# Kernel tuning notes

Hardware: AMD Instinct MI355X
Metric: run time of the kernel (lower is better)

Reference implementation:

```python
import jax, jax.numpy as jnp
import numpy as np

TAU = 0.07
EPS = 1e-12  # matches torch F.normalize clamp_min eps


def setup_inputs() -> dict:
    key = jax.random.key(0)
    k1, k2 = jax.random.split(key)
    feat = jax.random.normal(k1, (4, 64, 512, 512), dtype=jnp.float32)
    gt = jax.random.randint(k2, (4, 19, 512, 512), 0, 2, dtype=jnp.int32)
    return {"feat": feat, "gt": gt}


def reference(feat, gt):
    # feat: [b, c, h, w], gt: [b, k, h, w] multi-hot in {0,1}
    mask = (gt == 1).astype(feat.dtype)                      # [b,k,h,w]
    num_pos = mask.sum()

    # Scatter-sum class prototypes: k0[k] = sum of feat at positive pixels of class k
    k0 = jnp.einsum('bkhw,bchw->kc', mask, feat)             # [k,c]
    k0n = k0 / jnp.maximum(jnp.linalg.norm(k0, axis=1, keepdims=True), EPS)

    # Per-pixel L2-normalized features over channel dim
    fn = feat / jnp.maximum(jnp.linalg.norm(feat, axis=1, keepdims=True), EPS)

    # Cosine similarity to every prototype, temperature-scaled softmax NLL over classes
    logits = jnp.einsum('kc,bchw->bkhw', k0n, fn) / TAU      # [b,k,h,w]
    logp = jax.nn.log_softmax(logits, axis=1)

    # Sum NLL over all (pixel, class) positive pairs; a pixel positive for
    # multiple classes contributes once per class, exactly like the loop.
    loss = -(mask * logp).sum() / num_pos
    return loss
```

## Files before the change

### kernel.cpp

```cpp
#include <hip/hip_runtime.h>
#include <cstdint>
#include <cstddef>

#define HW    262144
#define C     64
#define K     19
#define NPIX  1048576
#define TAUINV (1.0f / 0.07f)
#define EPS   1e-12f

#define T1    128
#define NT1   (NPIX / T1)
#define TPB1  (HW / T1)
#define G1    2048


__device__ __forceinline__ float wave_reduce_f32(float v) {
#pragma unroll
    for (int off = 32; off; off >>= 1) v += __shfl_down(v, off);
    return v;
}

__device__ __forceinline__ unsigned wave_reduce_u32(unsigned v) {
#pragma unroll
    for (int off = 32; off; off >>= 1) v += __shfl_down(v, off);
    return v;
}

__device__ __forceinline__ void k1_prefetch(
    int tile, const float* __restrict__ feat, const int* __restrict__ gt,
    int tid, float4 f[8], unsigned* mpf)
{
    const int b   = tile >> 11;
    const int hw0 = (tile & (TPB1 - 1)) << 7;
    const float* fb = feat + (size_t)b * C * HW + hw0;
#pragma unroll
    for (int i = 0; i < 8; ++i) {
        const int v  = tid + (i << 8);
        const int c  = v >> 5;
        const int p0 = (v & 31) << 2;
        f[i] = *(const float4*)(fb + (size_t)c * HW + p0);
    }
    if (tid < T1) {
        const int* gp = gt + (size_t)b * K * HW + hw0 + tid;
        unsigned m = 0;
#pragma unroll
        for (int k = 0; k < K; ++k)
            m |= (gp[(size_t)k * HW] == 1) ? (1u << k) : 0u;
        *mpf = m;
    }
}

__global__ __launch_bounds__(256) void k1_proto(
    const float* __restrict__ feat, const int* __restrict__ gt,
    unsigned* __restrict__ pm,
    float* __restrict__ k0, unsigned* __restrict__ num_pos)
{
    __shared__ float    sf[64][129];
    __shared__ unsigned msk[T1];
    const int tid  = threadIdx.x;
    const int lane = tid & 63;
    const int wv   = tid >> 6;

    float acc[K];
#pragma unroll
    for (int k = 0; k < K; ++k) acc[k] = 0.0f;
    unsigned npos = 0;

    float4   f[8];
    unsigned mpf = 0;
    int tile = blockIdx.x;
    if (tile < NT1) k1_prefetch(tile, feat, gt, tid, f, &mpf);

    for (; tile < NT1; ) {
        if (tid < T1) {
            msk[tid] = mpf;
            if (pm) pm[(size_t)tile * T1 + tid] = mpf;
            npos += __popc(mpf);
        }
#pragma unroll
        for (int i = 0; i < 8; ++i) {
            const int v  = tid + (i << 8);
            const int c  = v >> 5;
            const int p0 = (v & 31) << 2;
            sf[c][p0 + 0] = f[i].x; sf[c][p0 + 1] = f[i].y;
            sf[c][p0 + 2] = f[i].z; sf[c][p0 + 3] = f[i].w;
        }
        __syncthreads();

        const int nxt = tile + G1;
        if (nxt < NT1) k1_prefetch(nxt, feat, gt, tid, f, &mpf);

#pragma unroll 4
        for (int p = 0; p < 32; ++p) {
            const int pp = (wv << 5) + p;
            const float    fv = sf[lane][pp];
            const unsigned m  = msk[pp];
#pragma unroll
            for (int k = 0; k < K; ++k) {
                const int s = ((int)(m << (31 - k))) >> 31;
                acc[k] += __int_as_float(s & __float_as_int(fv));
            }
        }
        __syncthreads();
        tile = nxt;
    }

    float* red = &sf[0][0];
    if (wv > 0) {
#pragma unroll
        for (int k = 0; k < K; ++k)
            red[(wv - 1) * (K * 64) + k * 64 + lane] = acc[k];
    }
    __syncthreads();
    if (wv == 0) {
#pragma unroll
        for (int k = 0; k < K; ++k) {
            const float v = acc[k]
                + red[0 * (K * 64) + k * 64 + lane]
                + red[1 * (K * 64) + k * 64 + lane]
                + red[2 * (K * 64) + k * 64 + lane];
            atomicAdd(&k0[k * 64 + lane], v);
        }
    }
    const unsigned np = wave_reduce_u32(npos);
    if (lane == 0) atomicAdd(num_pos, np);
}

__global__ __launch_bounds__(256) void k2_norm(
    const float* __restrict__ k0, float* __restrict__ k0n)
{
    __shared__ float rn[K];
    const int tid  = threadIdx.x;
    const int lane = tid & 63;
    const int wv   = tid >> 6;
    for (int cls = wv; cls < K; cls += 4) {
        const float v = k0[cls * 64 + lane];
        const float s = wave_reduce_f32(v * v);
        if (lane == 0) rn[cls] = 1.0f / fmaxf(sqrtf(s), EPS);
    }
    __syncthreads();
    for (int i = tid; i < K * 64; i += 256) k0n[i] = k0[i] * rn[i >> 6];
}

__global__ __launch_bounds__(256) void k3_loss(
    const float* __restrict__ feat, const int* __restrict__ gt,
    const unsigned* __restrict__ pm, const float* __restrict__ k0n,
    float* __restrict__ loss_sum)
{
    __shared__ __align__(16) float w[K * 64];
    const int tid = threadIdx.x;
    for (int i = tid; i < K * 64; i += 256) w[i] = k0n[i];
    __syncthreads();

    const int px0 = (blockIdx.x * 256 + tid) << 2;
    const int b   = px0 >> 18;
    const int hw  = px0 & (HW - 1);
    const float* fb = feat + (size_t)b * C * HW + hw;

    unsigned marr[4];
    if (pm) {
        const uint4 mv = *(const uint4*)(pm + px0);
        marr[0] = mv.x; marr[1] = mv.y; marr[2] = mv.z; marr[3] = mv.w;
    } else {
        marr[0] = marr[1] = marr[2] = marr[3] = 0;
        const int* gp = gt + (size_t)b * K * HW + hw;
#pragma unroll
        for (int k = 0; k < K; ++k) {
            const int4 g4 = *(const int4*)(gp + (size_t)k * HW);
            marr[0] |= (g4.x == 1) ? (1u << k) : 0u;
            marr[1] |= (g4.y == 1) ? (1u << k) : 0u;
            marr[2] |= (g4.z == 1) ? (1u << k) : 0u;
            marr[3] |= (g4.w == 1) ? (1u << k) : 0u;
        }
    }

    float4 dot[K];
#pragma unroll
    for (int k = 0; k < K; ++k) dot[k] = make_float4(0.f, 0.f, 0.f, 0.f);
    float4 ss = make_float4(0.f, 0.f, 0.f, 0.f);

    float4 f[8];
#pragma unroll
    for (int j = 0; j < 8; ++j)
        f[j] = *(const float4*)(fb + (size_t)j * HW);

#pragma unroll
    for (int cg = 0; cg < 64; cg += 8) {
        float4 g[8];
        if (cg + 8 < 64) {
#pragma unroll
            for (int j = 0; j < 8; ++j)
                g[j] = *(const float4*)(fb + (size_t)(cg + 8 + j) * HW);
        }
#pragma unroll
        for (int j = 0; j < 8; ++j) {
            const float4 fv = f[j];
            ss.x = fmaf(fv.x, fv.x, ss.x); ss.y = fmaf(fv.y, fv.y, ss.y);
            ss.z = fmaf(fv.z, fv.z, ss.z); ss.w = fmaf(fv.w, fv.w, ss.w);
        }
#pragma unroll
        for (int k = 0; k < K; ++k) {
            const float4 wa = *(const float4*)&w[k * 64 + cg];
            const float4 wb = *(const float4*)&w[k * 64 + cg + 4];
            float4 d = dot[k];
            d.x = fmaf(f[0].x, wa.x, d.x); d.y = fmaf(f[0].y, wa.x, d.y);
            d.z = fmaf(f[0].z, wa.x, d.z); d.w = fmaf(f[0].w, wa.x, d.w);
            d.x = fmaf(f[1].x, wa.y, d.x); d.y = fmaf(f[1].y, wa.y, d.y);
            d.z = fmaf(f[1].z, wa.y, d.z); d.w = fmaf(f[1].w, wa.y, d.w);
            d.x = fmaf(f[2].x, wa.z, d.x); d.y = fmaf(f[2].y, wa.z, d.y);
            d.z = fmaf(f[2].z, wa.z, d.z); d.w = fmaf(f[2].w, wa.z, d.w);
            d.x = fmaf(f[3].x, wa.w, d.x); d.y = fmaf(f[3].y, wa.w, d.y);
            d.z = fmaf(f[3].z, wa.w, d.z); d.w = fmaf(f[3].w, wa.w, d.w);
            d.x = fmaf(f[4].x, wb.x, d.x); d.y = fmaf(f[4].y, wb.x, d.y);
            d.z = fmaf(f[4].z, wb.x, d.z); d.w = fmaf(f[4].w, wb.x, d.w);
            d.x = fmaf(f[5].x, wb.y, d.x); d.y = fmaf(f[5].y, wb.y, d.y);
            d.z = fmaf(f[5].z, wb.y, d.z); d.w = fmaf(f[5].w, wb.y, d.w);
            d.x = fmaf(f[6].x, wb.z, d.x); d.y = fmaf(f[6].y, wb.z, d.y);
            d.z = fmaf(f[6].z, wb.z, d.z); d.w = fmaf(f[6].w, wb.z, d.w);
            d.x = fmaf(f[7].x, wb.w, d.x); d.y = fmaf(f[7].y, wb.w, d.y);
            d.z = fmaf(f[7].z, wb.w, d.z); d.w = fmaf(f[7].w, wb.w, d.w);
            dot[k] = d;
        }
        if (cg + 8 < 64) {
#pragma unroll
            for (int j = 0; j < 8; ++j) f[j] = g[j];
        }
    }

    float ls = 0.0f;
    float* dp = (float*)&dot[0];
    const float* sp = (const float*)&ss;
#pragma unroll
    for (int comp = 0; comp < 4; ++comp) {
        const float sc = TAUINV / fmaxf(sqrtf(sp[comp]), EPS);
        float mx = -1e30f;
#pragma unroll
        for (int k = 0; k < K; ++k) {
            dp[k * 4 + comp] *= sc;
            mx = fmaxf(mx, dp[k * 4 + comp]);
        }
        float se = 0.0f;
#pragma unroll
        for (int k = 0; k < K; ++k) se += expf(dp[k * 4 + comp] - mx);
        const float logZ = mx + logf(se);
        const unsigned m = marr[comp];
        ls += (float)__popc(m) * logZ;
#pragma unroll
        for (int k = 0; k < K; ++k) {
            const int s = ((int)(m << (31 - k))) >> 31;
            ls -= __int_as_float(s & __float_as_int(dp[k * 4 + comp]));
        }
    }

    ls = wave_reduce_f32(ls);
    if ((tid & 63) == 0) atomicAdd(loss_sum, ls);
}

__global__ void k4_final(const float* __restrict__ loss_sum,
                         const unsigned* __restrict__ num_pos,
                         float* __restrict__ out)
{
    out[0] = loss_sum[0] / (float)num_pos[0];
}

extern "C" void kernel_launch(void* const* d_in, const int* in_sizes, int n_in,
                              void* d_out, int out_size, void* d_ws, size_t ws_size,
                              hipStream_t stream)
{
    const float* feat = (const float*)d_in[0];
    const int*   gt   = (const int*)d_in[1];
    float*       out  = (float*)d_out;

    char* ws = (char*)d_ws;
    unsigned* num_pos  = (unsigned*)(ws + 0);
    float*    loss_sum = (float*)(ws + 4);
    float*    k0       = (float*)(ws + 64);
    float*    k0n      = (float*)(ws + 8192);
    unsigned* pm       = nullptr;
    if (ws_size >= 65536 + sizeof(unsigned) * (size_t)NPIX)
        pm = (unsigned*)(ws + 65536);

    hipMemsetAsync(d_ws, 0, 16384, stream);

    k1_proto<<<G1, 256, 0, stream>>>(feat, gt, pm, k0, num_pos);
    k2_norm <<<1,  256, 0, stream>>>(k0, k0n);
    k3_loss <<<NPIX / 1024, 256, 0, stream>>>(feat, gt, pm, k0n, loss_sum);
    k4_final<<<1, 1, 0, stream>>>(loss_sum, num_pos, out);
}
```

Before: 562.1 us.

## Compute class prototypes with bf16 MFMA using hi/lo split of features

The prototype scatter-sum kernel is rewritten so each wave takes 32-pixel chunks and computes the mask-by-feature product with 16x16x32 bf16 MFMA instructions. The masks become bf16 0/1 A operands, and each fp32 feature is split into high and low bf16 parts so the sum stays close to fp32. This replaces the scalar masked-add loop over 19 classes and the LDS transpose staging. The pixel-mask buffer is now always used, with no fallback when the workspace is small. This risks an out-of-bounds write if the workspace is too small and a small loss of precision from the two-term bf16 split.

Result: faster. 536.5 us (-4.5%).

```diff
diff --git a/kernel.cpp b/kernel.cpp
--- a/kernel.cpp
+++ b/kernel.cpp
@@ -9,138 +9,144 @@
 #define TAUINV (1.0f / 0.07f)
 #define EPS   1e-12f
 
-#define T1    128
-#define NT1   (NPIX / T1)
-#define TPB1  (HW / T1)
-#define G1    2048
-
+#define NCHUNK (NPIX / 32)
+#define CPB    8192
+#define G1     1024
+
+
+typedef __attribute__((ext_vector_type(8))) short bf16x8;
+typedef __attribute__((ext_vector_type(4))) float f32x4;
 
 __device__ __forceinline__ float wave_reduce_f32(float v) {
 #pragma unroll
     for (int off = 32; off; off >>= 1) v += __shfl_down(v, off);
     return v;
 }
-
 __device__ __forceinline__ unsigned wave_reduce_u32(unsigned v) {
 #pragma unroll
     for (int off = 32; off; off >>= 1) v += __shfl_down(v, off);
     return v;
 }
 
-__device__ __forceinline__ void k1_prefetch(
-    int tile, const float* __restrict__ feat, const int* __restrict__ gt,
-    int tid, float4 f[8], unsigned* mpf)
-{
-    const int b   = tile >> 11;
-    const int hw0 = (tile & (TPB1 - 1)) << 7;
-    const float* fb = feat + (size_t)b * C * HW + hw0;
-#pragma unroll
-    for (int i = 0; i < 8; ++i) {
-        const int v  = tid + (i << 8);
-        const int c  = v >> 5;
-        const int p0 = (v & 31) << 2;
-        f[i] = *(const float4*)(fb + (size_t)c * HW + p0);
-    }
-    if (tid < T1) {
-        const int* gp = gt + (size_t)b * K * HW + hw0 + tid;
-        unsigned m = 0;
-#pragma unroll
-        for (int k = 0; k < K; ++k)
-            m |= (gp[(size_t)k * HW] == 1) ? (1u << k) : 0u;
-        *mpf = m;
-    }
+__device__ __forceinline__ void split1(float f, short& h, short& l) {
+    const unsigned u  = __float_as_uint(f);
+    const unsigned hb = (u + 0x7FFFu + ((u >> 16) & 1u)) & 0xFFFF0000u;
+    h = (short)(hb >> 16);
+    const float lo = f - __uint_as_float(hb);
+    const unsigned v = __float_as_uint(lo);
+    l = (short)((v + 0x7FFFu + ((v >> 16) & 1u)) >> 16);
 }
 
 __global__ __launch_bounds__(256) void k1_proto(
     const float* __restrict__ feat, const int* __restrict__ gt,
     unsigned* __restrict__ pm,
-    float* __restrict__ k0, unsigned* __restrict__ num_pos)
-{
-    __shared__ float    sf[64][129];
-    __shared__ unsigned msk[T1];
+    float* __restrict__ k0p, unsigned* __restrict__ num_pos)
+{
+    __shared__ float red[32 * 64];
     const int tid  = threadIdx.x;
     const int lane = tid & 63;
     const int wv   = tid >> 6;
-
-    float acc[K];
-#pragma unroll
-    for (int k = 0; k < K; ++k) acc[k] = 0.0f;
+    const int q    = lane >> 4;
+    const int n    = lane & 15;
+    const int q8   = q << 3;
+
+    f32x4 acc[2][4];
+#pragma unroll
+    for (int mt = 0; mt < 2; ++mt)
+#pragma unroll
+        for (int nt = 0; nt < 4; ++nt)
+            acc[mt][nt] = (f32x4){0.f, 0.f, 0.f, 0.f};
     unsigned npos = 0;
 
-    float4   f[8];
-    unsigned mpf = 0;
-    int tile = blockIdx.x;
-    if (tile < NT1) k1_prefetch(tile, feat, gt, tid, f, &mpf);
-
-    for (; tile < NT1; ) {
-        if (tid < T1) {
-            msk[tid] = mpf;
-            if (pm) pm[(size_t)tile * T1 + tid] = mpf;
-            npos += __popc(mpf);
-        }
-#pragma unroll
-        for (int i = 0; i < 8; ++i) {
-            const int v  = tid + (i << 8);
-            const int c  = v >> 5;
-            const int p0 = (v & 31) << 2;
-            sf[c][p0 + 0] = f[i].x; sf[c][p0 + 1] = f[i].y;
-            sf[c][p0 + 2] = f[i].z; sf[c][p0 + 3] = f[i].w;
+    const int wave_id = blockIdx.x * 4 + wv;
+    const int nwaves  = G1 * 4;
+
+    for (int chunk = wave_id; chunk < NCHUNK; chunk += nwaves) {
+        const int b   = chunk >> 13;
+        const int hw0 = (chunk & (CPB - 1)) << 5;
+        const size_t fbase = (size_t)b * C * HW + hw0;
+
+        unsigned mymask = 0;
+        if (lane < 32) {
+            const int* gp = gt + (size_t)b * K * HW + hw0 + lane;
+#pragma unroll
+            for (int k = 0; k < K; ++k)
+                mymask |= (gp[(size_t)k * HW] == 1) ? (1u << k) : 0u;
+            pm[(size_t)chunk * 32 + lane] = mymask;
+            npos += __popc(mymask);
+        }
+
+        unsigned w8[8];
+#pragma unroll
+        for (int j = 0; j < 8; ++j) w8[j] = __shfl(mymask, q8 + j);
+        bf16x8 a0, a1;
+#pragma unroll
+        for (int j = 0; j < 8; ++j) {
+            a0[j] = (short)(((w8[j] >> n) & 1u) * 0x3F80u);
+            a1[j] = (short)(((w8[j] >> (n + 16)) & 1u) * 0x3F80u);
+        }
+
+        const float* fp = feat + fbase + (size_t)n * HW + q8;
+#pragma unroll
+        for (int nt = 0; nt < 4; ++nt) {
+            const float* p = fp + (size_t)(nt * 16) * HW;
+            const float4 x = *(const float4*)p;
+            const float4 y = *(const float4*)(p + 4);
+            bf16x8 bh, bl;
+            {
+                short h, l;
+                split1(x.x, h, l); bh[0] = h; bl[0] = l;
+                split1(x.y, h, l); bh[1] = h; bl[1] = l;
+                split1(x.z, h, l); bh[2] = h; bl[2] = l;
+                split1(x.w, h, l); bh[3] = h; bl[3] = l;
+                split1(y.x, h, l); bh[4] = h; bl[4] = l;
+                split1(y.y, h, l); bh[5] = h; bl[5] = l;
+                split1(y.z, h, l); bh[6] = h; bl[6] = l;
+                split1(y.w, h, l); bh[7] = h; bl[7] = l;
+            }
+            acc[0][nt] = __builtin_amdgcn_mfma_f32_16x16x32_bf16(a0, bh, acc[0][nt], 0, 0, 0);
+            acc[0][nt] = __builtin_amdgcn_mfma_f32_16x16x32_bf16(a0, bl, acc[0][nt], 0, 0, 0);
+            acc[1][nt] = __builtin_amdgcn_mfma_f32_16x16x32_bf16(a1, bh, acc[1][nt], 0, 0, 0);
+            acc[1][nt] = __builtin_amdgcn_mfma_f32_16x16x32_bf16(a1, bl, acc[1][nt], 0, 0, 0);
+        }
+    }
+
+    for (int w = 0; w < 4; ++w) {
+        if (wv == w) {
+#pragma unroll
+            for (int mt = 0; mt < 2; ++mt)
+#pragma unroll
+                for (int nt = 0; nt < 4; ++nt)
+#pragma unroll
+                    for (int r = 0; r < 4; ++r) {
+                        const int idx = (mt * 16 + q * 4 + r) * 64 + nt * 16 + n;
+                        if (w == 0) red[idx]  = acc[mt][nt][r];
+                        else        red[idx] += acc[mt][nt][r];
+                    }
         }
         __syncthreads();
-
-        const int nxt = tile + G1;
-        if (nxt < NT1) k1_prefetch(nxt, feat, gt, tid, f, &mpf);
-
-#pragma unroll 4
-        for (int p = 0; p < 32; ++p) {
-            const int pp = (wv << 5) + p;
-            const float    fv = sf[lane][pp];
-            const unsigned m  = msk[pp];
-#pragma unroll
-            for (int k = 0; k < K; ++k) {
-                const int s = ((int)(m << (31 - k))) >> 31;
-                acc[k] += __int_as_float(s & __float_as_int(fv));
-            }
-        }
-        __syncthreads();
-        tile = nxt;
-    }
-
-    float* red = &sf[0][0];
-    if (wv > 0) {
-#pragma unroll
-        for (int k = 0; k < K; ++k)
-            red[(wv - 1) * (K * 64) + k * 64 + lane] = acc[k];
-    }
-    __syncthreads();
-    if (wv == 0) {
-#pragma unroll
-        for (int k = 0; k < K; ++k) {
-            const float v = acc[k]
-                + red[0 * (K * 64) + k * 64 + lane]
-                + red[1 * (K * 64) + k * 64 + lane]
-                + red[2 * (K * 64) + k * 64 + lane];
-            atomicAdd(&k0[k * 64 + lane], v);
-        }
-    }
+    }
+    for (int i = tid; i < 32 * 64; i += 256)
+        atomicAdd(&k0p[i], red[i]);
+
     const unsigned np = wave_reduce_u32(npos);
     if (lane == 0) atomicAdd(num_pos, np);
 }
 
 __global__ __launch_bounds__(256) void k2_norm(
-    const float* __restrict__ k0, float* __restrict__ k0n)
+    const float* __restrict__ k0p, float* __restrict__ k0n)
 {
     __shared__ float rn[K];
     const int tid  = threadIdx.x;
     const int lane = tid & 63;
     const int wv   = tid >> 6;
     for (int cls = wv; cls < K; cls += 4) {
-        const float v = k0[cls * 64 + lane];
+        const float v = k0p[cls * 64 + lane];
         const float s = wave_reduce_f32(v * v);
         if (lane == 0) rn[cls] = 1.0f / fmaxf(sqrtf(s), EPS);
     }
     __syncthreads();
-    for (int i = tid; i < K * 64; i += 256) k0n[i] = k0[i] * rn[i >> 6];
+    for (int i = tid; i < K * 64; i += 256) k0n[i] = k0p[i] * rn[i >> 6];
 }
 
 __global__ __launch_bounds__(256) void k3_loss(
@@ -159,20 +165,9 @@
     const float* fb = feat + (size_t)b * C * HW + hw;
 
     unsigned marr[4];
-    if (pm) {
+    {
         const uint4 mv = *(const uint4*)(pm + px0);
         marr[0] = mv.x; marr[1] = mv.y; marr[2] = mv.z; marr[3] = mv.w;
-    } else {
-        marr[0] = marr[1] = marr[2] = marr[3] = 0;
-        const int* gp = gt + (size_t)b * K * HW + hw;
-#pragma unroll
-        for (int k = 0; k < K; ++k) {
-            const int4 g4 = *(const int4*)(gp + (size_t)k * HW);
-            marr[0] |= (g4.x == 1) ? (1u << k) : 0u;
-            marr[1] |= (g4.y == 1) ? (1u << k) : 0u;
-            marr[2] |= (g4.z == 1) ? (1u << k) : 0u;
-            marr[3] |= (g4.w == 1) ? (1u << k) : 0u;
-        }
     }
 
     float4 dot[K];
@@ -275,16 +270,14 @@
     char* ws = (char*)d_ws;
     unsigned* num_pos  = (unsigned*)(ws + 0);
     float*    loss_sum = (float*)(ws + 4);
-    float*    k0       = (float*)(ws + 64);
-    float*    k0n      = (float*)(ws + 8192);
-    unsigned* pm       = nullptr;
-    if (ws_size >= 65536 + sizeof(unsigned) * (size_t)NPIX)
-        pm = (unsigned*)(ws + 65536);
+    float*    k0p      = (float*)(ws + 256);
+    float*    k0n      = (float*)(ws + 8448);
+    unsigned* pm       = (unsigned*)(ws + 65536);
 
     hipMemsetAsync(d_ws, 0, 16384, stream);
 
-    k1_proto<<<G1, 256, 0, stream>>>(feat, gt, pm, k0, num_pos);
-    k2_norm <<<1,  256, 0, stream>>>(k0, k0n);
+    k1_proto<<<G1, 256, 0, stream>>>(feat, gt, pm, k0p, num_pos);
+    k2_norm <<<1,  256, 0, stream>>>(k0p, k0n);
     k3_loss <<<NPIX / 1024, 256, 0, stream>>>(feat, gt, pm, k0n, loss_sum);
     k4_final<<<1, 1, 0, stream>>>(loss_sum, num_pos, out);
 }
```
